# Kernel tuning notes

Measured on AMD Instinct MI355X. Metric: run time of the kernel, lower is better.

## Reference

```python
import jax, jax.numpy as jnp
import jax.lax as lax
import numpy as np

# ---- Parallel3DGeometry constants ----
B, C = 1, 1
D, H, W = 64, 96, 96          # internal volume layout (z, y, x)
V, U, A = 64, 96, 90          # detector rows, detector cols, projection angles
SX = SY = SD = 1.0            # voxel size (x, y, z)
SU = SV = 1.0                 # detector spacing
NSTEPS = H + W + 2            # upper bound on voxels crossed by an XY ray
DIAG = float(np.sqrt(SX * SX + SY * SY))
EPS = 1e-12


def _t_for(p0, dp, pmin, pmax):
    # slab entry/exit parameters, matching torch _t_for (incl. parallel-ray cases)
    par = jnp.abs(dp) < EPS
    safe = jnp.where(par, 1.0, dp)
    t0 = (pmin - p0) / safe
    t1 = (pmax - p0) / safe
    lo = jnp.minimum(t0, t1)
    hi = jnp.maximum(t0, t1)
    inside = (p0 >= pmin) & (p0 <= pmax)
    lo = jnp.where(par, jnp.where(inside, -jnp.inf, jnp.inf), lo)
    hi = jnp.where(par, jnp.where(inside, jnp.inf, -jnp.inf), hi)
    return lo, hi


def _trace():
    """Vectorized Siddon XY traversal for all A*U rays.

    Returns Is, Js (int32 [A,U,NSTEPS]) voxel indices and Ws (f32 [A,U,NSTEPS])
    segment lengths (0 where the ray has exited / padded steps).
    """
    angles = jnp.linspace(0.0, np.pi, A, endpoint=False).astype(jnp.float32)
    cos_t = jnp.cos(angles)
    sin_t = jnp.sin(angles)
    u = (jnp.arange(U, dtype=jnp.float32) - (U - 1) / 2.0) * SU
    dx = jnp.broadcast_to(cos_t[:, None], (A, U)).reshape(-1)
    dy = jnp.broadcast_to(sin_t[:, None], (A, U)).reshape(-1)
    x0 = (-u[None, :] * sin_t[:, None]).reshape(-1)
    y0 = (u[None, :] * cos_t[:, None]).reshape(-1)

    x_min = -((W - 1) / 2.0) * SX; x_max = ((W - 1) / 2.0) * SX
    y_min = -((H - 1) / 2.0) * SY; y_max = ((H - 1) / 2.0) * SY
    tx0, tx1 = _t_for(x0, dx, x_min, x_max)
    ty0, ty1 = _t_for(y0, dy, y_min, y_max)
    t_entry = jnp.maximum(tx0, ty0)
    t_exit = jnp.minimum(tx1, ty1)
    alive0 = t_entry < t_exit
    te = jnp.where(alive0, t_entry, 0.0)
    tex = jnp.where(alive0, t_exit, 0.0)
    xe = x0 + te * dx
    ye = y0 + te * dy
    i0 = jnp.clip(jnp.round(xe / SX + (W - 1) / 2.0), 0, W - 1).astype(jnp.int32)
    j0 = jnp.clip(jnp.round(ye / SY + (H - 1) / 2.0), 0, H - 1).astype(jnp.int32)
    cxw = (W - 1) / 2.0 * SX
    cyh = (H - 1) / 2.0 * SY

    def body(st, _):
        i, j, x, y, t, alive = st
        valid = alive & (t < tex - EPS)
        fi = i.astype(jnp.float32)
        fj = j.astype(jnp.float32)
        xn = jnp.where(dx > 0, (fi + 0.5) * SX - cxw,
                       jnp.where(dx < 0, (fi - 0.5) * SX - cxw, jnp.inf))
        yn = jnp.where(dy > 0, (fj + 0.5) * SY - cyh,
                       jnp.where(dy < 0, (fj - 0.5) * SY - cyh, jnp.inf))
        okx = jnp.abs(dx) > EPS
        oky = jnp.abs(dy) > EPS
        tx = jnp.where(okx, (xn - x) / jnp.where(okx, dx, 1.0), jnp.inf)
        ty = jnp.where(oky, (yn - y) / jnp.where(oky, dy, 1.0), jnp.inf)
        dt = jnp.minimum(jnp.minimum(tx, ty), tex - t)
        seg = jnp.maximum(0.0, dt * DIAG / jnp.maximum(jnp.abs(dx) + jnp.abs(dy), EPS))
        w = jnp.where(valid, seg, 0.0)
        i_n = i + jnp.where(tx <= ty, jnp.where(dx > 0, 1, -1), 0)
        j_n = j + jnp.where(ty <= tx, jnp.where(dy > 0, 1, -1), 0)
        inb = (i_n >= 0) & (i_n < W) & (j_n >= 0) & (j_n < H)
        dts = jnp.where(valid, dt, 0.0)
        st2 = (jnp.where(valid, i_n, i), jnp.where(valid, j_n, j),
               x + dx * dts, y + dy * dts, t + dts, valid & inb)
        return st2, (i, j, w)

    init = (i0, j0, xe, ye, te, alive0)
    _, (Is, Js, Ws) = lax.scan(body, init, None, length=NSTEPS)
    # [NSTEPS, R] -> [A, U, NSTEPS]
    Is = Is.T.reshape(A, U, NSTEPS)
    Js = Js.T.reshape(A, U, NSTEPS)
    Ws = Ws.T.reshape(A, U, NSTEPS)
    return Is, Js, Ws


def _forward(vol):
    # model-facing [B,C,X,Y,Z] -> internal [B,C,D,H,W]
    vol_int = jnp.transpose(vol, (0, 1, 4, 3, 2))
    Is, Js, Ws = _trace()
    v_phys = (jnp.arange(V, dtype=jnp.float32) - (V - 1) / 2.0) * SV
    k = jnp.clip(jnp.round(v_phys / SD + (D - 1) / 2.0), 0, D - 1).astype(jnp.int32)
    # gather voxel values along every ray: [B,C,V,A,U,NSTEPS]
    g = vol_int[:, :, k[:, None, None, None], Js[None], Is[None]]
    out = jnp.einsum('bcvaun,aun->bcvau', g, Ws.astype(vol.dtype))
    # internal [B,C,V,A,U] (== out[b,c,a,v,u] reordered) -> model-facing [B,C,U,A,V]
    return jnp.transpose(out, (0, 1, 4, 3, 2))


def setup_inputs() -> dict:
    key = jax.random.key(0)
    vol = jax.random.normal(key, (B, C, W, H, D), dtype=jnp.float32)
    return {"vol": vol}


def reference(vol):
    return _forward(vol)
```

## Files before the change

### kernel.cpp

```cpp
#include <hip/hip_runtime.h>
#include <math.h>

namespace {
constexpr int NA = 90, NU = 96, NV = 64, NW = 96, NH = 96, ND = 64;
constexpr int NRAY  = NA * NU;
constexpr int NENT  = 256;
constexpr int CNTMAX = 208;
constexpr int TILE  = 8;
constexpr int NBLK  = NRAY / TILE;
}

__global__ __launch_bounds__(512)
void siddon_fused(const float* __restrict__ vol, float* __restrict__ out)
{
    __shared__ int2 sEnt[TILE][NENT];
    __shared__ int  sCnt[TILE];

    const int tid  = threadIdx.x;
    const int wid  = tid >> 6;
    const int lane = tid & 63;
    const int tile = blockIdx.x;
    const int ray  = tile * TILE + wid;
    const int a    = ray / NU;
    const int u    = ray - a * NU;

    const float EPSf = 1e-12f;
    const float INFp = __builtin_inff();
    const float DIAG = 1.41421356237309514547f;

    const float ang = (float)a * (float)(3.14159265358979323846 / 90.0);
    const float dx = (float)cos((double)ang);
    const float dy = (float)sin((double)ang);
    const float uu = (float)u - 47.5f;
    const float x0 = __fmul_rn(-uu, dy);
    const float y0 = __fmul_rn( uu, dx);

    const float xmin = -47.5f, xmax = 47.5f;
    const float ymin = -47.5f, ymax = 47.5f;

    float tx0, tx1;
    {
        const bool par = fabsf(dx) < EPSf;
        const float safe = par ? 1.0f : dx;
        const float t0 = __fdiv_rn(xmin - x0, safe);
        const float t1 = __fdiv_rn(xmax - x0, safe);
        const float lo = fminf(t0, t1), hi = fmaxf(t0, t1);
        const bool inside = (x0 >= xmin) && (x0 <= xmax);
        tx0 = par ? (inside ? -INFp : INFp) : lo;
        tx1 = par ? (inside ?  INFp : -INFp) : hi;
    }
    float ty0, ty1;
    {
        const bool par = fabsf(dy) < EPSf;
        const float safe = par ? 1.0f : dy;
        const float t0 = __fdiv_rn(ymin - y0, safe);
        const float t1 = __fdiv_rn(ymax - y0, safe);
        const float lo = fminf(t0, t1), hi = fmaxf(t0, t1);
        const bool inside = (y0 >= ymin) && (y0 <= ymax);
        ty0 = par ? (inside ? -INFp : INFp) : lo;
        ty1 = par ? (inside ?  INFp : -INFp) : hi;
    }

    const float t_entry = fmaxf(tx0, ty0);
    const float t_exit  = fminf(tx1, ty1);
    const bool  alive0  = t_entry < t_exit;
    const float te  = alive0 ? t_entry : 0.0f;
    const float tex = alive0 ? t_exit  : 0.0f;

    const float xe = __fadd_rn(x0, __fmul_rn(te, dx));
    const float ye = __fadd_rn(y0, __fmul_rn(te, dy));
    const int i0 = (int)fminf(fmaxf(rintf(__fadd_rn(xe, 47.5f)), 0.0f), 95.0f);
    const int j0 = (int)fminf(fmaxf(rintf(__fadd_rn(ye, 47.5f)), 0.0f), 95.0f);

    const bool okx = fabsf(dx) > EPSf;
    const bool oky = fabsf(dy) > EPSf;
    const float inv_dx = okx ? __fdiv_rn(1.0f, dx) : 0.0f;
    const float inv_dy = oky ? __fdiv_rn(1.0f, dy) : 0.0f;
    const float wscale = __fdiv_rn(DIAG, fmaxf(fabsf(dx) + fabsf(dy), EPSf));
    const float tex_m_eps = __fadd_rn(tex, -EPSf);

    const float cx = (dx > 0.0f) ? -47.0f : -48.0f;
    const float cy = (dy > 0.0f) ? -47.0f : -48.0f;
    const float Ax = okx ? __fadd_rn(te, __fmul_rn(((float)i0 + cx) - xe, inv_dx)) : INFp;
    const float Ay = oky ? __fadd_rn(te, __fmul_rn(((float)j0 + cy) - ye, inv_dy)) : INFp;
    const float px = okx ? fabsf(inv_dx) : 0.0f;
    const float py = oky ? fabsf(inv_dy) : 0.0f;
    const int   si = (dx > 0.0f) ? 1 : -1;
    const int   sj = (dy > 0.0f) ? 1 : -1;

    const float inv_pq = __fdiv_rn(1.0f, px + py);
    const float Cc = Ay - Ax;

    int2* __restrict__ myRow = &sEnt[wid][0];
    int cnt = 0;
    #pragma unroll
    for (int rnd = 0; rnd < 4; ++rnd) {
        const int n = (rnd << 6) + lane;
        const float nf = (float)n;

        float kf = __fmul_rn(__fmaf_rn(nf, py, Cc), inv_pq);
        kf = fminf(fmaxf(kf, 0.0f), nf);
        int k = (int)rintf(kf);

        #pragma unroll
        for (int it = 0; it < 4; ++it) {
            const int m = n - k;
            const float Txk   = __fmaf_rn((float)k, px, Ax);
            const float Txkm1 = (k > 0) ? __fmaf_rn((float)(k - 1), px, Ax) : -INFp;
            const float Tyl   = __fmaf_rn((float)m, py, Ay);
            const float Tylm1 = (m > 0) ? __fmaf_rn((float)(m - 1), py, Ay) : -INFp;
            const bool dec = (Txkm1 > Tyl);
            const bool inc = (!dec) && (Tylm1 > Txk);
            k += inc ? 1 : (dec ? -1 : 0);
        }

        const int m = n - k;
        const float Txk   = __fmaf_rn((float)k, px, Ax);
        const float Txkm1 = (k > 0) ? __fmaf_rn((float)(k - 1), px, Ax) : -INFp;
        const float Tyl   = __fmaf_rn((float)m, py, Ay);
        const float Tylm1 = (m > 0) ? __fmaf_rn((float)(m - 1), py, Ay) : -INFp;

        const float Tn   = fminf(Txk, Tyl);
        const float prev = fmaxf(te, fmaxf(Txkm1, Tylm1));
        const float dt   = __fadd_rn(fminf(Tn, tex), -fminf(prev, tex));
        const bool active = alive0 && (prev < tex_m_eps);
        float w = __fmul_rn(fmaxf(0.0f, dt), wscale);
        w = active ? w : 0.0f;

        const int ii = min(95, max(0, i0 + ((si > 0) ? k : -k)));
        const int jj = min(95, max(0, j0 + ((sj > 0) ? m : -m)));
        int2 e;
        e.x = (ii * NH + jj) << 8;
        e.y = __float_as_int(w);
        myRow[n] = e;

        cnt += (int)__popcll(__ballot(active));
    }
    if (lane == 0) sCnt[wid] = min((cnt + 15) & ~15, CNTMAX);
    __syncthreads();

    const int r   = lane >> 4;
    const int sub = lane & 15;
    const int subOff = sub << 4;

    const int cap = sCnt[wid];
    const int2* __restrict__ eRow = &sEnt[wid][r];
    const char* __restrict__ vb   = (const char*)vol;

    float4 aA = {0,0,0,0}, aB = {0,0,0,0}, aC = {0,0,0,0}, aD = {0,0,0,0};
    for (int n = 0; n < cap; n += 16) {
        const int2 e0 = eRow[n];
        const int2 e1 = eRow[n + 4];
        const int2 e2 = eRow[n + 8];
        const int2 e3 = eRow[n + 12];
        const float w0 = __int_as_float(e0.y);
        const float w1 = __int_as_float(e1.y);
        const float w2 = __int_as_float(e2.y);
        const float w3 = __int_as_float(e3.y);
        const float4 v0 = *(const float4*)(vb + (e0.x + subOff));
        const float4 v1 = *(const float4*)(vb + (e1.x + subOff));
        const float4 v2 = *(const float4*)(vb + (e2.x + subOff));
        const float4 v3 = *(const float4*)(vb + (e3.x + subOff));
        aA.x = fmaf(w0, v0.x, aA.x); aA.y = fmaf(w0, v0.y, aA.y);
        aA.z = fmaf(w0, v0.z, aA.z); aA.w = fmaf(w0, v0.w, aA.w);
        aB.x = fmaf(w1, v1.x, aB.x); aB.y = fmaf(w1, v1.y, aB.y);
        aB.z = fmaf(w1, v1.z, aB.z); aB.w = fmaf(w1, v1.w, aB.w);
        aC.x = fmaf(w2, v2.x, aC.x); aC.y = fmaf(w2, v2.y, aC.y);
        aC.z = fmaf(w2, v2.z, aC.z); aC.w = fmaf(w2, v2.w, aC.w);
        aD.x = fmaf(w3, v3.x, aD.x); aD.y = fmaf(w3, v3.y, aD.y);
        aD.z = fmaf(w3, v3.z, aD.z); aD.w = fmaf(w3, v3.w, aD.w);
    }
    float sx = (aA.x + aB.x) + (aC.x + aD.x);
    float sy = (aA.y + aB.y) + (aC.y + aD.y);
    float sz = (aA.z + aB.z) + (aC.z + aD.z);
    float sw = (aA.w + aB.w) + (aC.w + aD.w);

    sx += __shfl_xor(sx, 16, 64);  sy += __shfl_xor(sy, 16, 64);
    sz += __shfl_xor(sz, 16, 64);  sw += __shfl_xor(sw, 16, 64);
    sx += __shfl_xor(sx, 32, 64);  sy += __shfl_xor(sy, 32, 64);
    sz += __shfl_xor(sz, 32, 64);  sw += __shfl_xor(sw, 32, 64);

    if (lane < 16) {
        float4 res; res.x = sx; res.y = sy; res.z = sz; res.w = sw;
        *(float4*)(out + (u * NA + a) * NV + (sub << 2)) = res;
    }
}

extern "C" void kernel_launch(void* const* d_in, const int* in_sizes, int n_in,
                              void* d_out, int out_size, void* d_ws, size_t ws_size,
                              hipStream_t stream) {
    const float* vol = (const float*)d_in[0];
    float* out = (float*)d_out;
    hipLaunchKernelGGL(siddon_fused, dim3(NBLK), dim3(512), 0, stream, vol, out);
}
```

Baseline: 70.41 us.

## Convert volume to fp16 in workspace and gather half-precision z-rows

Adds a pre-pass kernel that converts the float volume to fp16 in the workspace. The main kernel then gathers 16-byte chunks holding 8 halves, so each z-row takes 8 lanes instead of 16, and each wave processes 8 entries per step instead of 4. This halves gather bytes and instruction count in the accumulation loop. In exchange it adds a second launch and reduced input precision, which may exceed the tolerance, and it raises the entry cap and padding granularity.

```diff
diff --git a/kernel.cpp b/kernel.cpp
--- a/kernel.cpp
+++ b/kernel.cpp
@@ -3,15 +3,27 @@
 
 namespace {
 constexpr int NA = 90, NU = 96, NV = 64, NW = 96, NH = 96, ND = 64;
-constexpr int NRAY  = NA * NU;
-constexpr int NENT  = 256;
-constexpr int CNTMAX = 208;
-constexpr int TILE  = 8;
-constexpr int NBLK  = NRAY / TILE;
+constexpr int NRAY   = NA * NU;
+constexpr int NVOX   = NW * NH * ND;
+constexpr int NENT   = 256;
+constexpr int CNTMAX = 224;
+constexpr int TILE   = 8;
+constexpr int NBLK   = NRAY / TILE;
+typedef _Float16 f16_t;
+}
+
+__global__ __launch_bounds__(256)
+void vol_to_f16(const float* __restrict__ vol, f16_t* __restrict__ v16)
+{
+    const int idx = (blockIdx.x * 256 + threadIdx.x) * 4;
+    const float4 f = *(const float4*)(vol + idx);
+    f16_t h[4];
+    h[0] = (f16_t)f.x; h[1] = (f16_t)f.y; h[2] = (f16_t)f.z; h[3] = (f16_t)f.w;
+    *(ushort4*)(v16 + idx) = *(const ushort4*)h;
 }
 
 __global__ __launch_bounds__(512)
-void siddon_fused(const float* __restrict__ vol, float* __restrict__ out)
+void siddon_fused(const f16_t* __restrict__ v16, float* __restrict__ out)
 {
     __shared__ int2 sEnt[TILE][NENT];
     __shared__ int  sCnt[TILE];
@@ -130,59 +142,50 @@
         const int ii = min(95, max(0, i0 + ((si > 0) ? k : -k)));
         const int jj = min(95, max(0, j0 + ((sj > 0) ? m : -m)));
         int2 e;
-        e.x = (ii * NH + jj) << 8;
+        e.x = (ii * NH + jj) << 7;
         e.y = __float_as_int(w);
         myRow[n] = e;
 
         cnt += (int)__popcll(__ballot(active));
     }
-    if (lane == 0) sCnt[wid] = min((cnt + 15) & ~15, CNTMAX);
+    if (lane == 0) sCnt[wid] = min((cnt + 31) & ~31, CNTMAX);
     __syncthreads();
 
-    const int r   = lane >> 4;
-    const int sub = lane & 15;
+    const int r   = lane >> 3;
+    const int sub = lane & 7;
     const int subOff = sub << 4;
 
     const int cap = sCnt[wid];
     const int2* __restrict__ eRow = &sEnt[wid][r];
-    const char* __restrict__ vb   = (const char*)vol;
-
-    float4 aA = {0,0,0,0}, aB = {0,0,0,0}, aC = {0,0,0,0}, aD = {0,0,0,0};
-    for (int n = 0; n < cap; n += 16) {
-        const int2 e0 = eRow[n];
-        const int2 e1 = eRow[n + 4];
-        const int2 e2 = eRow[n + 8];
-        const int2 e3 = eRow[n + 12];
-        const float w0 = __int_as_float(e0.y);
-        const float w1 = __int_as_float(e1.y);
-        const float w2 = __int_as_float(e2.y);
-        const float w3 = __int_as_float(e3.y);
-        const float4 v0 = *(const float4*)(vb + (e0.x + subOff));
-        const float4 v1 = *(const float4*)(vb + (e1.x + subOff));
-        const float4 v2 = *(const float4*)(vb + (e2.x + subOff));
-        const float4 v3 = *(const float4*)(vb + (e3.x + subOff));
-        aA.x = fmaf(w0, v0.x, aA.x); aA.y = fmaf(w0, v0.y, aA.y);
-        aA.z = fmaf(w0, v0.z, aA.z); aA.w = fmaf(w0, v0.w, aA.w);
-        aB.x = fmaf(w1, v1.x, aB.x); aB.y = fmaf(w1, v1.y, aB.y);
-        aB.z = fmaf(w1, v1.z, aB.z); aB.w = fmaf(w1, v1.w, aB.w);
-        aC.x = fmaf(w2, v2.x, aC.x); aC.y = fmaf(w2, v2.y, aC.y);
-        aC.z = fmaf(w2, v2.z, aC.z); aC.w = fmaf(w2, v2.w, aC.w);
-        aD.x = fmaf(w3, v3.x, aD.x); aD.y = fmaf(w3, v3.y, aD.y);
-        aD.z = fmaf(w3, v3.z, aD.z); aD.w = fmaf(w3, v3.w, aD.w);
-    }
-    float sx = (aA.x + aB.x) + (aC.x + aD.x);
-    float sy = (aA.y + aB.y) + (aC.y + aD.y);
-    float sz = (aA.z + aB.z) + (aC.z + aD.z);
-    float sw = (aA.w + aB.w) + (aC.w + aD.w);
-
-    sx += __shfl_xor(sx, 16, 64);  sy += __shfl_xor(sy, 16, 64);
-    sz += __shfl_xor(sz, 16, 64);  sw += __shfl_xor(sw, 16, 64);
-    sx += __shfl_xor(sx, 32, 64);  sy += __shfl_xor(sy, 32, 64);
-    sz += __shfl_xor(sz, 32, 64);  sw += __shfl_xor(sw, 32, 64);
-
-    if (lane < 16) {
-        float4 res; res.x = sx; res.y = sy; res.z = sz; res.w = sw;
-        *(float4*)(out + (u * NA + a) * NV + (sub << 2)) = res;
+    const char* __restrict__ vb   = (const char*)v16;
+
+    float acc[8] = {0, 0, 0, 0, 0, 0, 0, 0};
+    for (int n = 0; n < cap; n += 32) {
+        #pragma unroll
+        for (int b = 0; b < 4; ++b) {
+            const int2 e = eRow[n + b * 8];
+            const float w = __int_as_float(e.y);
+            const uint4 q = *(const uint4*)(vb + (e.x + subOff));
+            const f16_t* h = (const f16_t*)&q;
+            #pragma unroll
+            for (int k = 0; k < 8; ++k)
+                acc[k] = fmaf(w, (float)h[k], acc[k]);
+        }
+    }
+
+    #pragma unroll
+    for (int k = 0; k < 8; ++k) {
+        acc[k] += __shfl_xor(acc[k], 8, 64);
+        acc[k] += __shfl_xor(acc[k], 16, 64);
+        acc[k] += __shfl_xor(acc[k], 32, 64);
+    }
+
+    if (lane < 8) {
+        float* dst = out + (u * NA + a) * NV + (sub << 3);
+        float4 lo; lo.x = acc[0]; lo.y = acc[1]; lo.z = acc[2]; lo.w = acc[3];
+        float4 hi; hi.x = acc[4]; hi.y = acc[5]; hi.z = acc[6]; hi.w = acc[7];
+        *(float4*)dst = lo;
+        *(float4*)(dst + 4) = hi;
     }
 }
 
@@ -191,5 +194,7 @@
                               hipStream_t stream) {
     const float* vol = (const float*)d_in[0];
     float* out = (float*)d_out;
-    hipLaunchKernelGGL(siddon_fused, dim3(NBLK), dim3(512), 0, stream, vol, out);
-}
+    f16_t* v16 = (f16_t*)d_ws;
+    hipLaunchKernelGGL(vol_to_f16, dim3(NVOX / 4 / 256), dim3(256), 0, stream, vol, v16);
+    hipLaunchKernelGGL(siddon_fused, dim3(NBLK), dim3(512), 0, stream, v16, out);
+}
```

Result: slower. 73.76 us (+4.8%).
